# Optimization experiments

Hardware: AMD Instinct MI355X
Metric: run time of the kernel (lower is better)

## Reference

```python
import jax, jax.numpy as jnp
import numpy as np

B, D, H, W, C = 1, 16, 56, 56, 256
NH = 8
WS = (8, 7, 7)
SS = (4, 3, 3)
HID = 4 * C
N = WS[0] * WS[1] * WS[2]          # 392 tokens per window
SCALE = (C // NH) ** -0.5
TBL = (2 * WS[0] - 1) * (2 * WS[1] - 1) * (2 * WS[2] - 1)  # 2535


def _rel_pos_index():
    cd, ch, cw = [np.arange(w) for w in WS]
    coords = np.stack(np.meshgrid(cd, ch, cw, indexing='ij')).reshape(3, -1)  # (3, N)
    rel = (coords[:, :, None] - coords[:, None, :]).transpose(1, 2, 0)        # (N, N, 3)
    rel[:, :, 0] += WS[0] - 1
    rel[:, :, 1] += WS[1] - 1
    rel[:, :, 2] += WS[2] - 1
    rel[:, :, 0] *= (2 * WS[1] - 1) * (2 * WS[2] - 1)
    rel[:, :, 1] *= 2 * WS[2] - 1
    return rel.sum(-1)  # (N, N) int

REL_IDX = _rel_pos_index()


def _partition(x):
    # (b, D, H, W, c) -> (b*nW, N, c)
    b, c = x.shape[0], x.shape[-1]
    x = x.reshape(b, D // WS[0], WS[0], H // WS[1], WS[1], W // WS[2], WS[2], c)
    return x.transpose(0, 1, 3, 5, 2, 4, 6, 7).reshape(-1, N, c)


def _reverse(wins, b):
    # (b*nW, N, c) -> (b, D, H, W, c)
    x = wins.reshape(b, D // WS[0], H // WS[1], W // WS[2], WS[0], WS[1], WS[2], -1)
    return x.transpose(0, 1, 4, 2, 5, 3, 6, 7).reshape(b, D, H, W, -1)


def _attn_mask():
    # standard Swin cyclic-shift mask, computed once on host (static shapes)
    img = np.zeros((1, D, H, W, 1), dtype=np.float32)
    cnt = 0
    for ds in (slice(0, -WS[0]), slice(-WS[0], -SS[0]), slice(-SS[0], None)):
        for hs in (slice(0, -WS[1]), slice(-WS[1], -SS[1]), slice(-SS[1], None)):
            for ws_ in (slice(0, -WS[2]), slice(-WS[2], -SS[2]), slice(-SS[2], None)):
                img[:, ds, hs, ws_, :] = cnt
                cnt += 1
    mw = _partition(img).squeeze(-1)               # (nW, N)
    am = mw[:, None, :] - mw[:, :, None]           # (nW, N, N)
    return np.where(am != 0, np.float32(-100.0), np.float32(0.0))

ATTN_MASK = _attn_mask()  # (nW, N, N)


def _ln(x, g, b):
    m = x.mean(-1, keepdims=True)
    v = x.var(-1, keepdims=True)
    return (x - m) * jax.lax.rsqrt(v + 1e-5) * g + b


def _fwd(x, norm1_g, norm1_b, qkv_w, qkv_b, rel_bias, proj_w, proj_b,
         norm2_g, norm2_b, fc1_w, fc1_b, fc2_w, fc2_b):
    shortcut = x
    h = _ln(x, norm1_g, norm1_b)
    h = jnp.roll(h, (-SS[0], -SS[1], -SS[2]), axis=(1, 2, 3))
    wins = _partition(h)                                    # (B*nW, N, C)
    qkv = wins @ qkv_w.T + qkv_b                            # (B*nW, N, 3C)
    qkv = qkv.reshape(-1, N, 3, NH, C // NH).transpose(2, 0, 3, 1, 4)
    q, k, v = qkv[0] * SCALE, qkv[1], qkv[2]                # (B*nW, NH, N, d)
    attn = jnp.einsum('bhnd,bhmd->bhnm', q, k)              # (B*nW, NH, N, N)
    bias = rel_bias[REL_IDX.reshape(-1)].reshape(N, N, NH).transpose(2, 0, 1)
    attn = attn + bias[None]
    nW = attn.shape[0] // B
    attn = attn.reshape(B, nW, NH, N, N) + jnp.asarray(ATTN_MASK)[None, :, None]
    attn = jax.nn.softmax(attn.reshape(-1, NH, N, N), axis=-1)
    out = jnp.einsum('bhnm,bhmd->bhnd', attn, v)            # (B*nW, NH, N, d)
    out = out.transpose(0, 2, 1, 3).reshape(-1, N, C)
    out = out @ proj_w.T + proj_b
    h = _reverse(out, B)
    h = jnp.roll(h, SS, axis=(1, 2, 3))
    x = shortcut + h
    y = _ln(x, norm2_g, norm2_b)
    y = jax.nn.gelu(y @ fc1_w.T + fc1_b, approximate=False)
    y = y @ fc2_w.T + fc2_b
    return x + y


def setup_inputs() -> dict:
    key = jax.random.key(0)
    ks = jax.random.split(key, 6)
    return {
        'x': jax.random.normal(ks[0], (B, D, H, W, C), dtype=jnp.float32),
        'norm1_g': jnp.ones((C,), jnp.float32),
        'norm1_b': jnp.zeros((C,), jnp.float32),
        'qkv_w': jax.random.normal(ks[1], (3 * C, C), jnp.float32) * 0.02,
        'qkv_b': jnp.zeros((3 * C,), jnp.float32),
        'rel_bias': jax.random.normal(ks[2], (TBL, NH), jnp.float32) * 0.02,
        'proj_w': jax.random.normal(ks[3], (C, C), jnp.float32) * 0.02,
        'proj_b': jnp.zeros((C,), jnp.float32),
        'norm2_g': jnp.ones((C,), jnp.float32),
        'norm2_b': jnp.zeros((C,), jnp.float32),
        'fc1_w': jax.random.normal(ks[4], (HID, C), jnp.float32) * 0.02,
        'fc1_b': jnp.zeros((HID,), jnp.float32),
        'fc2_w': jax.random.normal(ks[5], (C, HID), jnp.float32) * 0.02,
        'fc2_b': jnp.zeros((C,), jnp.float32),
    }


def reference(x, norm1_g, norm1_b, qkv_w, qkv_b, rel_bias, proj_w, proj_b,
              norm2_g, norm2_b, fc1_w, fc1_b, fc2_w, fc2_b):
    return _fwd(x, norm1_g, norm1_b, qkv_w, qkv_b, rel_bias, proj_w, proj_b,
                norm2_g, norm2_b, fc1_w, fc1_b, fc2_w, fc2_b)
```

## Files before the change

### kernel.cpp

```cpp
#include <hip/hip_runtime.h>
#include <hip/hip_bf16.h>

typedef unsigned char u8;
typedef unsigned short u16;
typedef unsigned int u32;
typedef float f32x2 __attribute__((ext_vector_type(2)));
typedef float f32x4 __attribute__((ext_vector_type(4)));
typedef short bf16x8 __attribute__((ext_vector_type(8)));
typedef short bf16x4 __attribute__((ext_vector_type(4)));
typedef unsigned int u32x4 __attribute__((ext_vector_type(4)));

#define NTOK 392
#define CDIM 256
#define TOKS 50176
#define BKP  400
#define VTP  408
#define LOG2E 1.4426950408889634f

__device__ __forceinline__ u16 f2b(float x) {
  union { __hip_bfloat16 b; u16 u; } cv; cv.b = __float2bfloat16(x); return cv.u;
}
__device__ __forceinline__ float exp2_fast(float x) {
#if __has_builtin(__builtin_amdgcn_exp2f)
  return __builtin_amdgcn_exp2f(x);
#else
  float r; asm("v_exp_f32 %0, %1" : "=v"(r) : "v"(x)); return r;
#endif
}

__device__ __forceinline__ u8 f2e4m3(float x) {
  float ax = fabsf(x);
  u32 s = (x < 0.f) ? 0x80u : 0u;
  if (ax >= 448.f) return (u8)(s | 0x7E);
  int e; float m = frexpf(ax, &e);
  int E = e - 1;
  if (E < -6) {
    int q = (int)rintf(ax * 512.f);
    return (u8)(s | q);
  }
  int q = (int)rintf(m * 16.f) - 8;
  if (q == 8) { q = 0; E += 1; if (E > 8) return (u8)(s | 0x7E); }
  return (u8)(s | ((E + 7) << 3) | q);
}
__device__ __forceinline__ float e4m3f(u32 b) {
  u32 s = (b & 0x80u) << 24;
  u32 e = (b >> 3) & 15u, m = b & 7u;
  if (e) { union { u32 u; float f; } c; c.u = s | ((e + 120u) << 23) | (m << 20); return c.f; }
  float v = (float)m * 0x1p-9f;
  return s ? -v : v;
}
__device__ __forceinline__ void fp8x4_to_f32x4(u32 w, f32x4* out) {
#if __has_builtin(__builtin_amdgcn_cvt_pk_f32_fp8)
  f32x2 lo = __builtin_amdgcn_cvt_pk_f32_fp8(w, false);
  f32x2 hi = __builtin_amdgcn_cvt_pk_f32_fp8(w, true);
  (*out)[0] = lo[0]; (*out)[1] = lo[1]; (*out)[2] = hi[0]; (*out)[3] = hi[1];
#else
  (*out)[0] = e4m3f(w & 255); (*out)[1] = e4m3f((w >> 8) & 255);
  (*out)[2] = e4m3f((w >> 16) & 255); (*out)[3] = e4m3f(w >> 24);
#endif
}

__device__ __forceinline__ f32x4 mfma16(bf16x4 a, bf16x4 b, f32x4 c) {
#if __has_builtin(__builtin_amdgcn_mfma_f32_16x16x16bf16_1k)
  return __builtin_amdgcn_mfma_f32_16x16x16bf16_1k(a, b, c, 0, 0, 0);
#else
  asm volatile("v_mfma_f32_16x16x16_bf16 %0, %1, %2, %0"
               : "+v"(c) : "v"(a), "v"(b));
  return c;
#endif
}

__global__ void conv_kernel(const float* __restrict__ in, u16* __restrict__ out, int n) {
  int i = blockIdx.x * 256 + threadIdx.x;
  if (i < n) out[i] = f2b(in[i]);
}

__global__ __launch_bounds__(256) void ln_kernel(const float* __restrict__ x,
    const float* __restrict__ g, const float* __restrict__ b,
    u16* __restrict__ out, int permute) {
  const int t = blockIdx.x * 4 + (threadIdx.x >> 6), lane = threadIdx.x & 63;
  size_t src;
  if (permute) {
    int w = t / NTOK, n = t % NTOK;
    int wd = w >> 6, wh = (w >> 3) & 7, ww = w & 7;
    int td = n / 49, rr = n % 49, th = rr / 7, tw = rr % 7;
    int d  = (wd * 8 + td + 4) & 15;
    int hh = (wh * 7 + th + 3) % 56;
    int wc = (ww * 7 + tw + 3) % 56;
    src = ((size_t)((d * 56 + hh) * 56 + wc)) * CDIM;
  } else {
    src = (size_t)t * CDIM;
  }
  f32x4 v = *(const f32x4*)(x + src + lane * 4);
  float s  = v[0] + v[1] + v[2] + v[3];
  float s2 = v[0]*v[0] + v[1]*v[1] + v[2]*v[2] + v[3]*v[3];
  #pragma unroll
  for (int o = 1; o < 64; o <<= 1) { s += __shfl_xor(s, o); s2 += __shfl_xor(s2, o); }
  float mean = s * (1.f / CDIM);
  float var  = s2 * (1.f / CDIM) - mean * mean;
  float rs   = rsqrtf(var + 1e-5f);
  f32x4 gg = *(const f32x4*)(g + lane * 4);
  f32x4 bb = *(const f32x4*)(b + lane * 4);
  bf16x4 o4;
  #pragma unroll
  for (int j = 0; j < 4; ++j) o4[j] = (short)f2b((v[j] - mean) * rs * gg[j] + bb[j]);
  *(bf16x4*)(out + (size_t)t * CDIM + lane * 4) = o4;
}

__global__ void mb_kernel(const float* __restrict__ rel, u8* __restrict__ mb) {
  int idx = blockIdx.x * 256 + threadIdx.x;
  if (idx >= 8 * NTOK * BKP) return;
  int pat = idx / (NTOK * BKP);
  int r   = idx % (NTOK * BKP);
  int q = r / BKP, k = r % BKP;
  int pd = (pat >> 2) & 1, ph = (pat >> 1) & 1, pw = pat & 1;
  if (k >= NTOK) {
    #pragma unroll
    for (int h = 0; h < 8; ++h)
      mb[((size_t)(pat * 8 + h) * NTOK + q) * BKP + k] = 0xFE;
    return;
  }
  int td = q / 49, th = (q % 49) / 7, tw = q % 7;
  int md = k / 49, mh = (k % 49) / 7, mw = k % 7;
  int cq = (pd ? (td < 4 ? 1 : 2) : 0) * 9 + (ph ? (th < 4 ? 1 : 2) : 0) * 3 + (pw ? (tw < 4 ? 1 : 2) : 0);
  int ck = (pd ? (md < 4 ? 1 : 2) : 0) * 9 + (ph ? (mh < 4 ? 1 : 2) : 0) * 3 + (pw ? (mw < 4 ? 1 : 2) : 0);
  float mask = (cq == ck) ? 0.f : -100.f;
  int ridx = (td - md + 7) * 169 + (th - mh + 6) * 13 + (tw - mw + 6);
  const float* rp = rel + (size_t)ridx * 8;
  #pragma unroll
  for (int h = 0; h < 8; ++h)
    mb[((size_t)(pat * 8 + h) * NTOK + q) * BKP + k] = f2e4m3((rp[h] + mask) * LOG2E);
}

template<class Epi>
__global__ __launch_bounds__(256, 2) void gemm_bt(const u16* __restrict__ A,
    const u16* __restrict__ B, int K, int nx, Epi epi) {
  __shared__ __align__(16) u16 As[128 * 64];
  __shared__ __align__(16) u16 Bs[128 * 64];
  const int nwg = gridDim.x;
  const int q8 = nwg >> 3, r8 = nwg & 7;
  const int xcd = blockIdx.x & 7, bix = blockIdx.x >> 3;
  const int logical = (xcd < r8) ? (xcd * (q8 + 1) + bix)
                                 : (r8 * (q8 + 1) + (xcd - r8) * q8 + bix);
  const int bm = (logical / nx) * 128, bn = (logical % nx) * 128;
  const int tid = threadIdx.x, lane = tid & 63, wv = tid >> 6;
  const int wm = (wv >> 1) * 64, wn = (wv & 1) * 64;
  const int l16 = lane & 15, g = lane >> 4;
  const int sw = l16 & 7;
  const int srow = (lane >> 3);
  const int scc  = (lane & 7) ^ srow;
  f32x4 acc[4][4];
  #pragma unroll
  for (int i = 0; i < 4; ++i)
    #pragma unroll
    for (int j = 0; j < 4; ++j) acc[i][j] = (f32x4){0.f, 0.f, 0.f, 0.f};
  for (int k0 = 0; k0 < K; k0 += 64) {
    #pragma unroll
    for (int c = 0; c < 4; ++c) {
      int row = wv * 32 + c * 8 + srow;
      const u16* ga = A + (size_t)(bm + row) * K + k0 + scc * 8;
      const u16* gb = B + (size_t)(bn + row) * K + k0 + scc * 8;
      __builtin_amdgcn_global_load_lds(
          (const __attribute__((address_space(1))) void*)ga,
          (__attribute__((address_space(3))) void*)(As + (wv * 32 + c * 8) * 64), 16, 0, 0);
      __builtin_amdgcn_global_load_lds(
          (const __attribute__((address_space(1))) void*)gb,
          (__attribute__((address_space(3))) void*)(Bs + (wv * 32 + c * 8) * 64), 16, 0, 0);
    }
    __syncthreads();
    #pragma unroll
    for (int kk = 0; kk < 2; ++kk) {
      bf16x8 fa[4], fb[4];
      #pragma unroll
      for (int i = 0; i < 4; ++i)
        fa[i] = *(const bf16x8*)(As + (wm + i * 16 + l16) * 64 + (((kk * 4 + g) ^ sw) * 8));
      #pragma unroll
      for (int i = 0; i < 4; ++i)
        fb[i] = *(const bf16x8*)(Bs + (wn + i * 16 + l16) * 64 + (((kk * 4 + g) ^ sw) * 8));
      #pragma unroll
      for (int mi = 0; mi < 4; ++mi)
        #pragma unroll
        for (int ni = 0; ni < 4; ++ni)
          acc[mi][ni] = __builtin_amdgcn_mfma_f32_16x16x32_bf16(fb[ni], fa[mi], acc[mi][ni], 0, 0, 0);
    }
    __syncthreads();
  }
  #pragma unroll
  for (int mi = 0; mi < 4; ++mi) {
    const int row = bm + wm + mi * 16 + l16;
    #pragma unroll
    for (int ni = 0; ni < 4; ++ni)
      epi(row, bn + wn + ni * 16 + g * 4, acc[mi][ni]);
  }
}

struct EpiQKV {
  const float* __restrict__ qb;
  u16 *q, *k, *v;
  __device__ void operator()(int row, int col, f32x4 val) const {
    f32x4 b4 = *(const f32x4*)(qb + col);
    int which = col >> 8, hd = col & 255;
    int head = hd >> 5, d = hd & 31;
    int w = row / NTOK, n = row - w * NTOK;
    if (which == 2) {
      u16* p = v + (((size_t)w * 8 + head) * 32 + d) * NTOK + n;
      #pragma unroll
      for (int j = 0; j < 4; ++j) p[(size_t)j * NTOK] = f2b(val[j] + b4[j]);
    } else {
      const float sc = (which == 0) ? 0.17677669529663687f * LOG2E : 1.f;
      bf16x4 o;
      #pragma unroll
      for (int j = 0; j < 4; ++j) o[j] = (short)f2b((val[j] + b4[j]) * sc);
      u16* p = (which == 0 ? q : k) + (((size_t)w * 8 + head) * NTOK + n) * 32 + d;
      *(bf16x4*)p = o;
    }
  }
};

struct EpiProj {
  const float* __restrict__ pb;
  const float* __restrict__ x;
  float* xr;
  __device__ void operator()(int row, int col, f32x4 val) const {
    f32x4 b4 = *(const f32x4*)(pb + col);
    int w = row / NTOK, n = row - w * NTOK;
    int wd = w >> 6, wh = (w >> 3) & 7, ww = w & 7;
    int td = n / 49, rr = n % 49, th = rr / 7, tw = rr % 7;
    int d  = (wd * 8 + td + 4) & 15;
    int hh = (wh * 7 + th + 3) % 56;
    int wc = (ww * 7 + tw + 3) % 56;
    size_t t = ((size_t)((d * 56 + hh) * 56 + wc)) * CDIM + col;
    f32x4 xv = *(const f32x4*)(x + t);
    f32x4 o;
    #pragma unroll
    for (int j = 0; j < 4; ++j) o[j] = xv[j] + val[j] + b4[j];
    *(f32x4*)(xr + t) = o;
  }
};

struct EpiFC1 {
  const float* __restrict__ fb;
  u16* y;
  __device__ void operator()(int row, int col, f32x4 val) const {
    f32x4 b4 = *(const f32x4*)(fb + col);
    bf16x4 o;
    #pragma unroll
    for (int j = 0; j < 4; ++j) {
      float u = val[j] + b4[j];
      u = 0.5f * u * (1.0f + erff(u * 0.70710678118654752f));
      o[j] = (short)f2b(u);
    }
    *(bf16x4*)(y + (size_t)row * 1024 + col) = o;
  }
};

struct EpiFC2 {
  const float* __restrict__ fb;
  const float* __restrict__ xr;
  float* out;
  __device__ void operator()(int row, int col, f32x4 val) const {
    f32x4 b4 = *(const f32x4*)(fb + col);
    size_t t = (size_t)row * CDIM + col;
    f32x4 xv = *(const f32x4*)(xr + t);
    f32x4 o;
    #pragma unroll
    for (int j = 0; j < 4; ++j) o[j] = xv[j] + val[j] + b4[j];
    *(f32x4*)(out + t) = o;
  }
};

__global__ __launch_bounds__(256, 2) void attn_kernel(
    const u16* __restrict__ qb, const u16* __restrict__ kb,
    const u16* __restrict__ vb, const u8* __restrict__ mb,
    u16* __restrict__ out) {
  __shared__ __align__(16) u16 Ks[25 * 512];
  __shared__ __align__(16) u16 Vt[32 * VTP];
  __shared__ __align__(16) u8  Ms[64 * BKP];
  const int h = blockIdx.x & 7;
  const int r = blockIdx.x >> 3;
  const int cum[9] = {0, 49, 56, 63, 64, 113, 120, 127, 128};
  int pat = 0;
  #pragma unroll
  for (int p = 0; p < 8; ++p) pat += (r >= cum[p + 1]) ? 1 : 0;
  const int i = r - cum[pat];
  const int pd = (pat >> 2) & 1, ph = (pat >> 1) & 1, pw = pat & 1;
  const int nw = pw ? 1 : 7;
  const int wh = ph ? 7 : i / nw;
  const int ww = pw ? 7 : i % nw;
  const int w = pd * 64 + wh * 8 + ww;

  const int tid = threadIdx.x, lane = tid & 63, wv = tid >> 6;
  const size_t base = (size_t)(w * 8 + h) * (NTOK * 32);
  const u8* mplane = mb + (size_t)(pat * 8 + h) * NTOK * BKP;

  for (int idx = tid; idx < 32 * 16; idx += 256)
    Vt[(idx >> 4) * VTP + NTOK + (idx & 15)] = 0;
  for (int c = tid; c < 400 * 4; c += 256) {
    int rr = c >> 2, cb = c & 3;
    int rs = rr < NTOK ? rr : NTOK - 1;
    *(bf16x8*)(Ks + (rr >> 4) * 512 + cb * 128 + (rr & 15) * 8) =
        *(const bf16x8*)(kb + base + (size_t)rs * 32 + cb * 8);
  }
  for (int c = tid; c < 32 * 49; c += 256) {
    int d = c / 49, ch = c % 49;
    *(bf16x8*)(Vt + d * VTP + ch * 8) =
        *(const bf16x8*)(vb + base + (size_t)d * NTOK + ch * 8);
  }

  u32x4 pf[7];
  #pragma unroll
  for (int j = 0; j < 7; ++j) {
    int idx = tid + j * 256;
    if (idx < 1600) {
      int row = idx / 25, cb = idx % 25;
      pf[j] = *(const u32x4*)(mplane + (size_t)row * BKP + cb * 16);
    }
  }

  const int l16 = lane & 15, g = lane >> 4;
  for (int round = 0; round < 7; ++round) {
    #pragma unroll
    for (int j = 0; j < 7; ++j) {
      int idx = tid + j * 256;
      if (idx < 1600) {
        int row = idx / 25, cb = idx % 25;
        *(u32x4*)(Ms + row * BKP + cb * 16) = pf[j];
      }
    }
    if (round < 6) {
      #pragma unroll
      for (int j = 0; j < 7; ++j) {
        int idx = tid + j * 256;
        if (idx < 1600) {
          int row = idx / 25, cb = idx % 25;
          int qrow = (round + 1) * 64 + row; qrow = qrow < NTOK ? qrow : NTOK - 1;
          pf[j] = *(const u32x4*)(mplane + (size_t)qrow * BKP + cb * 16);
        }
      }
    }
    __syncthreads();
    const int qt = round * 4 + wv;
    if (qt < 25) {
      const int qq = qt * 16 + l16;
      const int qc = qq < NTOK ? qq : NTOK - 1;
      const bf16x8 qf = *(const bf16x8*)(qb + base + (size_t)qc * 32 + g * 8);
      const u8* mrow = Ms + (wv * 16 + l16) * BKP + 4 * g;
      f32x4 o00 = {0.f,0.f,0.f,0.f}, o01 = {0.f,0.f,0.f,0.f};
      f32x4 o10 = {0.f,0.f,0.f,0.f}, o11 = {0.f,0.f,0.f,0.f};
      float psum = 0.f;
      #pragma unroll
      for (int t = 0; t < 25; ++t) {
        bf16x8 kf = *(const bf16x8*)(Ks + t * 512 + g * 128 + l16 * 8);
        u32 mw = *(const u32*)(mrow + t * 16);
        f32x4 c;
        fp8x4_to_f32x4(mw, &c);
        f32x4 st = __builtin_amdgcn_mfma_f32_16x16x32_bf16(kf, qf, c, 0, 0, 0);
        float p0 = exp2_fast(st[0]), p1 = exp2_fast(st[1]);
        float p2 = exp2_fast(st[2]), p3 = exp2_fast(st[3]);
        psum += (p0 + p1) + (p2 + p3);
        bf16x4 pfv;
        pfv[0] = (short)f2b(p0); pfv[1] = (short)f2b(p1);
        pfv[2] = (short)f2b(p2); pfv[3] = (short)f2b(p3);
        bf16x4 v0 = *(const bf16x4*)(Vt + l16 * VTP + t * 16 + 4 * g);
        bf16x4 v1 = *(const bf16x4*)(Vt + (16 + l16) * VTP + t * 16 + 4 * g);
        if (t & 1) { o01 = mfma16(v0, pfv, o01); o11 = mfma16(v1, pfv, o11); }
        else       { o00 = mfma16(v0, pfv, o00); o10 = mfma16(v1, pfv, o10); }
      }
      psum += __shfl_xor(psum, 16);
      psum += __shfl_xor(psum, 32);
      if (qq < NTOK) {
        float inv = 1.f / psum;
        bf16x4 w0, w1;
        #pragma unroll
        for (int j = 0; j < 4; ++j) {
          w0[j] = (short)f2b((o00[j] + o01[j]) * inv);
          w1[j] = (short)f2b((o10[j] + o11[j]) * inv);
        }
        u16* op = out + ((size_t)(w * NTOK + qq)) * CDIM + h * 32;
        *(bf16x4*)(op + 4 * g) = w0;
        *(bf16x4*)(op + 16 + 4 * g) = w1;
      }
    }
    __syncthreads();
  }
}

extern "C" void kernel_launch(void* const* d_in, const int* in_sizes, int n_in,
                              void* d_out, int out_size, void* d_ws, size_t ws_size,
                              hipStream_t stream) {
  const float* x      = (const float*)d_in[0];
  const float* n1g    = (const float*)d_in[1];
  const float* n1b    = (const float*)d_in[2];
  const float* qkv_w  = (const float*)d_in[3];
  const float* qkv_b  = (const float*)d_in[4];
  const float* rel    = (const float*)d_in[5];
  const float* proj_w = (const float*)d_in[6];
  const float* proj_b = (const float*)d_in[7];
  const float* n2g    = (const float*)d_in[8];
  const float* n2b    = (const float*)d_in[9];
  const float* fc1_w  = (const float*)d_in[10];
  const float* fc1_b  = (const float*)d_in[11];
  const float* fc2_w  = (const float*)d_in[12];
  const float* fc2_b  = (const float*)d_in[13];
  float* out = (float*)d_out;
  char* ws = (char*)d_ws;

  const size_t PL = (size_t)TOKS * CDIM * 2;
  const size_t MBSZ = (size_t)8 * 8 * NTOK * BKP;
  u16*   wins = (u16*)(ws);
  u16*   aout = (u16*)(ws + PL);
  u8*    mbuf = (u8*)(ws + 2 * PL);
  u16*   qbuf = (u16*)(ws + 2 * PL + MBSZ);
  u16*   kbuf = (u16*)(ws + 4 * PL);
  u16*   vbuf = (u16*)(ws + 5 * PL);
  float* xres = (float*)(ws + 4 * PL);
  u16*   h2   = (u16*)(ws + 6 * PL);
  u16*   wq   = (u16*)(ws + 7 * PL);
  u16*   wp   = wq + 768 * 256;
  u16*   w1   = wp + 256 * 256;
  u16*   w2   = w1 + 1024 * 256;
  u16*   y1   = (u16*)(ws);

  conv_kernel<<<768, 256, 0, stream>>>(qkv_w, wq, 196608);
  conv_kernel<<<256, 256, 0, stream>>>(proj_w, wp, 65536);
  conv_kernel<<<1024, 256, 0, stream>>>(fc1_w, w1, 262144);
  conv_kernel<<<1024, 256, 0, stream>>>(fc2_w, w2, 262144);
  mb_kernel<<<(8 * NTOK * BKP + 255) / 256, 256, 0, stream>>>(rel, mbuf);
  ln_kernel<<<TOKS / 4, 256, 0, stream>>>(x, n1g, n1b, wins, 1);
  gemm_bt<<<2352, 256, 0, stream>>>(wins, wq, 256, 6, EpiQKV{qkv_b, qbuf, kbuf, vbuf});
  attn_kernel<<<1024, 256, 0, stream>>>(qbuf, kbuf, vbuf, mbuf, aout);
  gemm_bt<<<784, 256, 0, stream>>>(aout, wp, 256, 2, EpiProj{proj_b, x, xres});
  ln_kernel<<<TOKS / 4, 256, 0, stream>>>(xres, n2g, n2b, h2, 0);
  gemm_bt<<<3136, 256, 0, stream>>>(h2, w1, 256, 8, EpiFC1{fc1_b, y1});
  gemm_bt<<<784, 256, 0, stream>>>(y1, w2, 1024, 2, EpiFC2{fc2_b, xres, out});
}
```

Before: 281.4 us.

## Store residual in bf16, fuse weight conversions, read K directly from global in attention

Merges the four weight-conversion launches into one kernel. Stores the post-attention residual as bf16 instead of fp32, which halves its write and read traffic in the proj epilogue, the second LayerNorm and the FC2 epilogue, at some cost in residual precision. Drops the K shared-memory staging in attention and loads K fragments straight from global memory. This frees LDS so occupancy can rise to 3 blocks per CU, but it relies on cache hits for the repeated K reads across waves.

```diff
diff --git a/kernel.cpp b/kernel.cpp
--- a/kernel.cpp
+++ b/kernel.cpp
@@ -19,6 +19,9 @@
 
 __device__ __forceinline__ u16 f2b(float x) {
   union { __hip_bfloat16 b; u16 u; } cv; cv.b = __float2bfloat16(x); return cv.u;
+}
+__device__ __forceinline__ float b2f(u16 u) {
+  union { unsigned int i; float f; } c; c.i = ((unsigned int)u) << 16; return c.f;
 }
 __device__ __forceinline__ float exp2_fast(float x) {
 #if __has_builtin(__builtin_amdgcn_exp2f)
@@ -70,28 +73,53 @@
 #endif
 }
 
-__global__ void conv_kernel(const float* __restrict__ in, u16* __restrict__ out, int n) {
+__global__ void wconv_kernel(const float* __restrict__ a, const float* __restrict__ b,
+                             const float* __restrict__ c, const float* __restrict__ d,
+                             u16* __restrict__ out) {
   int i = blockIdx.x * 256 + threadIdx.x;
-  if (i < n) out[i] = f2b(in[i]);
-}
-
-__global__ __launch_bounds__(256) void ln_kernel(const float* __restrict__ x,
+  const float* src; int off;
+  if (i < 196608)      { src = a; off = i; }
+  else if (i < 262144) { src = b; off = i - 196608; }
+  else if (i < 524288) { src = c; off = i - 262144; }
+  else                 { src = d; off = i - 524288; }
+  out[i] = f2b(src[off]);
+}
+
+__global__ __launch_bounds__(256) void ln1_kernel(const float* __restrict__ x,
     const float* __restrict__ g, const float* __restrict__ b,
-    u16* __restrict__ out, int permute) {
+    u16* __restrict__ out) {
   const int t = blockIdx.x * 4 + (threadIdx.x >> 6), lane = threadIdx.x & 63;
-  size_t src;
-  if (permute) {
-    int w = t / NTOK, n = t % NTOK;
-    int wd = w >> 6, wh = (w >> 3) & 7, ww = w & 7;
-    int td = n / 49, rr = n % 49, th = rr / 7, tw = rr % 7;
-    int d  = (wd * 8 + td + 4) & 15;
-    int hh = (wh * 7 + th + 3) % 56;
-    int wc = (ww * 7 + tw + 3) % 56;
-    src = ((size_t)((d * 56 + hh) * 56 + wc)) * CDIM;
-  } else {
-    src = (size_t)t * CDIM;
-  }
+  int w = t / NTOK, n = t % NTOK;
+  int wd = w >> 6, wh = (w >> 3) & 7, ww = w & 7;
+  int td = n / 49, rr = n % 49, th = rr / 7, tw = rr % 7;
+  int d  = (wd * 8 + td + 4) & 15;
+  int hh = (wh * 7 + th + 3) % 56;
+  int wc = (ww * 7 + tw + 3) % 56;
+  size_t src = ((size_t)((d * 56 + hh) * 56 + wc)) * CDIM;
   f32x4 v = *(const f32x4*)(x + src + lane * 4);
+  float s  = v[0] + v[1] + v[2] + v[3];
+  float s2 = v[0]*v[0] + v[1]*v[1] + v[2]*v[2] + v[3]*v[3];
+  #pragma unroll
+  for (int o = 1; o < 64; o <<= 1) { s += __shfl_xor(s, o); s2 += __shfl_xor(s2, o); }
+  float mean = s * (1.f / CDIM);
+  float var  = s2 * (1.f / CDIM) - mean * mean;
+  float rs   = rsqrtf(var + 1e-5f);
+  f32x4 gg = *(const f32x4*)(g + lane * 4);
+  f32x4 bb = *(const f32x4*)(b + lane * 4);
+  bf16x4 o4;
+  #pragma unroll
+  for (int j = 0; j < 4; ++j) o4[j] = (short)f2b((v[j] - mean) * rs * gg[j] + bb[j]);
+  *(bf16x4*)(out + (size_t)t * CDIM + lane * 4) = o4;
+}
+
+__global__ __launch_bounds__(256) void ln2_kernel(const u16* __restrict__ x,
+    const float* __restrict__ g, const float* __restrict__ b,
+    u16* __restrict__ out) {
+  const int t = blockIdx.x * 4 + (threadIdx.x >> 6), lane = threadIdx.x & 63;
+  bf16x4 v4 = *(const bf16x4*)(x + (size_t)t * CDIM + lane * 4);
+  f32x4 v;
+  #pragma unroll
+  for (int j = 0; j < 4; ++j) v[j] = b2f((u16)v4[j]);
   float s  = v[0] + v[1] + v[2] + v[3];
   float s2 = v[0]*v[0] + v[1]*v[1] + v[2]*v[2] + v[3]*v[3];
   #pragma unroll
@@ -220,7 +248,7 @@
 struct EpiProj {
   const float* __restrict__ pb;
   const float* __restrict__ x;
-  float* xr;
+  u16* xr;
   __device__ void operator()(int row, int col, f32x4 val) const {
     f32x4 b4 = *(const f32x4*)(pb + col);
     int w = row / NTOK, n = row - w * NTOK;
@@ -231,10 +259,10 @@
     int wc = (ww * 7 + tw + 3) % 56;
     size_t t = ((size_t)((d * 56 + hh) * 56 + wc)) * CDIM + col;
     f32x4 xv = *(const f32x4*)(x + t);
-    f32x4 o;
-    #pragma unroll
-    for (int j = 0; j < 4; ++j) o[j] = xv[j] + val[j] + b4[j];
-    *(f32x4*)(xr + t) = o;
+    bf16x4 o;
+    #pragma unroll
+    for (int j = 0; j < 4; ++j) o[j] = (short)f2b(xv[j] + val[j] + b4[j]);
+    *(bf16x4*)(xr + t) = o;
   }
 };
 
@@ -256,24 +284,23 @@
 
 struct EpiFC2 {
   const float* __restrict__ fb;
-  const float* __restrict__ xr;
+  const u16* __restrict__ xr;
   float* out;
   __device__ void operator()(int row, int col, f32x4 val) const {
     f32x4 b4 = *(const f32x4*)(fb + col);
     size_t t = (size_t)row * CDIM + col;
-    f32x4 xv = *(const f32x4*)(xr + t);
+    bf16x4 xv = *(const bf16x4*)(xr + t);
     f32x4 o;
     #pragma unroll
-    for (int j = 0; j < 4; ++j) o[j] = xv[j] + val[j] + b4[j];
+    for (int j = 0; j < 4; ++j) o[j] = b2f((u16)xv[j]) + val[j] + b4[j];
     *(f32x4*)(out + t) = o;
   }
 };
 
-__global__ __launch_bounds__(256, 2) void attn_kernel(
+__global__ __launch_bounds__(256, 3) void attn_kernel(
     const u16* __restrict__ qb, const u16* __restrict__ kb,
     const u16* __restrict__ vb, const u8* __restrict__ mb,
     u16* __restrict__ out) {
-  __shared__ __align__(16) u16 Ks[25 * 512];
   __shared__ __align__(16) u16 Vt[32 * VTP];
   __shared__ __align__(16) u8  Ms[64 * BKP];
   const int h = blockIdx.x & 7;
@@ -295,12 +322,6 @@
 
   for (int idx = tid; idx < 32 * 16; idx += 256)
     Vt[(idx >> 4) * VTP + NTOK + (idx & 15)] = 0;
-  for (int c = tid; c < 400 * 4; c += 256) {
-    int rr = c >> 2, cb = c & 3;
-    int rs = rr < NTOK ? rr : NTOK - 1;
-    *(bf16x8*)(Ks + (rr >> 4) * 512 + cb * 128 + (rr & 15) * 8) =
-        *(const bf16x8*)(kb + base + (size_t)rs * 32 + cb * 8);
-  }
   for (int c = tid; c < 32 * 49; c += 256) {
     int d = c / 49, ch = c % 49;
     *(bf16x8*)(Vt + d * VTP + ch * 8) =
@@ -350,7 +371,8 @@
       float psum = 0.f;
       #pragma unroll
       for (int t = 0; t < 25; ++t) {
-        bf16x8 kf = *(const bf16x8*)(Ks + t * 512 + g * 128 + l16 * 8);
+        int kr = t * 16 + l16; kr = kr < NTOK ? kr : NTOK - 1;
+        bf16x8 kf = *(const bf16x8*)(kb + base + (size_t)kr * 32 + g * 8);
         u32 mw = *(const u32*)(mrow + t * 16);
         f32x4 c;
         fp8x4_to_f32x4(mw, &c);
@@ -413,24 +435,18 @@
   u16*   qbuf = (u16*)(ws + 2 * PL + MBSZ);
   u16*   kbuf = (u16*)(ws + 4 * PL);
   u16*   vbuf = (u16*)(ws + 5 * PL);
-  float* xres = (float*)(ws + 4 * PL);
+  u16*   xres = (u16*)(ws + 4 * PL);
   u16*   h2   = (u16*)(ws + 6 * PL);
   u16*   wq   = (u16*)(ws + 7 * PL);
-  u16*   wp   = wq + 768 * 256;
-  u16*   w1   = wp + 256 * 256;
-  u16*   w2   = w1 + 1024 * 256;
   u16*   y1   = (u16*)(ws);
 
-  conv_kernel<<<768, 256, 0, stream>>>(qkv_w, wq, 196608);
-  conv_kernel<<<256, 256, 0, stream>>>(proj_w, wp, 65536);
-  conv_kernel<<<1024, 256, 0, stream>>>(fc1_w, w1, 262144);
-  conv_kernel<<<1024, 256, 0, stream>>>(fc2_w, w2, 262144);
+  wconv_kernel<<<3072, 256, 0, stream>>>(qkv_w, proj_w, fc1_w, fc2_w, wq);
   mb_kernel<<<(8 * NTOK * BKP + 255) / 256, 256, 0, stream>>>(rel, mbuf);
-  ln_kernel<<<TOKS / 4, 256, 0, stream>>>(x, n1g, n1b, wins, 1);
+  ln1_kernel<<<TOKS / 4, 256, 0, stream>>>(x, n1g, n1b, wins);
   gemm_bt<<<2352, 256, 0, stream>>>(wins, wq, 256, 6, EpiQKV{qkv_b, qbuf, kbuf, vbuf});
   attn_kernel<<<1024, 256, 0, stream>>>(qbuf, kbuf, vbuf, mbuf, aout);
-  gemm_bt<<<784, 256, 0, stream>>>(aout, wp, 256, 2, EpiProj{proj_b, x, xres});
-  ln_kernel<<<TOKS / 4, 256, 0, stream>>>(xres, n2g, n2b, h2, 0);
-  gemm_bt<<<3136, 256, 0, stream>>>(h2, w1, 256, 8, EpiFC1{fc1_b, y1});
-  gemm_bt<<<784, 256, 0, stream>>>(y1, w2, 1024, 2, EpiFC2{fc2_b, xres, out});
-}
+  gemm_bt<<<784, 256, 0, stream>>>(aout, wq + 196608, 256, 2, EpiProj{proj_b, x, xres});
+  ln2_kernel<<<TOKS / 4, 256, 0, stream>>>(xres, n2g, n2b, h2);
+  gemm_bt<<<3136, 256, 0, stream>>>(h2, wq + 262144, 256, 8, EpiFC1{fc1_b, y1});
+  gemm_bt<<<784, 256, 0, stream>>>(y1, wq + 524288, 1024, 2, EpiFC2{fc2_b, xres, out});
+}
```

Result: slower. 321.7 us (+14.3%).
